# Performance work log

Hardware: AMD Instinct MI355X
Metric: run time of the kernel (lower is better)

Reference implementation:

```python
import jax, jax.numpy as jnp
import numpy as np

D_MODEL = 512
N_HEAD = 8
D_HEAD = D_MODEL // N_HEAD


def setup_inputs() -> dict:
    key = jax.random.key(0)
    ks = jax.random.split(key, 8)
    B, S, T = 4, 512, 32
    src = jax.random.normal(ks[0], (B, S, D_MODEL), dtype=jnp.float32)
    tgt = jax.random.normal(ks[1], (B, S, T, D_MODEL), dtype=jnp.float32)
    tgt_padding_mask = jax.random.bernoulli(ks[2], 0.1, (B, S, T))
    scale = 1.0 / np.sqrt(D_MODEL)
    in_proj_weight = jax.random.uniform(ks[3], (3 * D_MODEL, D_MODEL), dtype=jnp.float32, minval=-scale, maxval=scale)
    in_proj_bias = jnp.zeros((3 * D_MODEL,), dtype=jnp.float32)
    out_proj_weight = jax.random.uniform(ks[4], (D_MODEL, D_MODEL), dtype=jnp.float32, minval=-scale, maxval=scale)
    out_proj_bias = jnp.zeros((D_MODEL,), dtype=jnp.float32)
    return {
        "src": src,
        "tgt": tgt,
        "tgt_padding_mask": tgt_padding_mask,
        "in_proj_weight": in_proj_weight,
        "in_proj_bias": in_proj_bias,
        "out_proj_weight": out_proj_weight,
        "out_proj_bias": out_proj_bias,
    }


def reference(src, tgt, tgt_padding_mask, in_proj_weight, in_proj_bias, out_proj_weight, out_proj_bias):
    # KNN-style cross attention branch (tgt is [B, S, T, D]).
    B, S, _ = src.shape
    T = tgt.shape[-2]
    w_src, w_tgt = in_proj_weight[:D_MODEL], in_proj_weight[D_MODEL:]
    b_src, b_tgt = in_proj_bias[:D_MODEL], in_proj_bias[D_MODEL:]

    q = src @ w_src.T + b_src                      # [B, S, D]
    kv = tgt @ w_tgt.T + b_tgt                     # [B, S, T, 2D]
    k, v = kv[..., :D_MODEL], kv[..., D_MODEL:]

    # mask handling: drop the mask for queries with no valid tgt, zero them later
    attn_invalid = tgt_padding_mask                # [B, S, T]
    mask_no_tgt_valid = jnp.all(attn_invalid, axis=-1)           # [B, S]
    attn_invalid = attn_invalid & ~mask_no_tgt_valid[..., None]

    q = q.reshape(B, S, N_HEAD, D_HEAD)            # [B, S, H, Dh]
    k = k.reshape(B, S, T, N_HEAD, D_HEAD)
    v = v.reshape(B, S, T, N_HEAD, D_HEAD)

    attn = jnp.einsum("bshd,bsthd->bhst", q, k)    # [B, H, S, T]
    attn = jnp.where(attn_invalid[:, None], -jnp.inf, attn)
    attn = jax.nn.softmax(attn / jnp.sqrt(jnp.asarray(D_HEAD, attn.dtype)), axis=-1)

    out = jnp.einsum("bhst,bsthd->bshd", attn, v).reshape(B, S, D_MODEL)
    out = out @ out_proj_weight.T + out_proj_bias
    out = jnp.where(mask_no_tgt_valid[..., None], 0.0, out)
    return out
```

## Files before the change

### kernel.cpp

```cpp
#include <hip/hip_runtime.h>
#include <hip/hip_bf16.h>

#define BS_   2048
#define T_    32
#define DM_   512

typedef __attribute__((ext_vector_type(8))) short frag8;
typedef __attribute__((ext_vector_type(4))) float f32x4;

__device__ __forceinline__ short f2s(float v) {
    return __builtin_bit_cast(short, __float2bfloat16(v));
}
__device__ __forceinline__ float s2f(short x) {
    return __builtin_bit_cast(float, (unsigned)(unsigned short)x << 16);
}
__device__ __forceinline__ void stv(float* p, float v)          { *p = v; }
__device__ __forceinline__ void stv(__hip_bfloat16* p, float v) { *p = __float2bfloat16(v); }

__device__ __forceinline__ void gl_lds16(const __hip_bfloat16* g, __hip_bfloat16* l) {
    __builtin_amdgcn_global_load_lds(
        (const __attribute__((address_space(1))) unsigned int*)g,
        (__attribute__((address_space(3))) unsigned int*)l, 16, 0, 0);
}

__global__ __launch_bounds__(256)
void prep(const float* __restrict__ ipw, const float* __restrict__ opw,
          const float* __restrict__ src,
          __hip_bfloat16* __restrict__ ipw_bf, __hip_bfloat16* __restrict__ opw_bf,
          __hip_bfloat16* __restrict__ src_bf, __hip_bfloat16* __restrict__ Tk)
{
    __shared__ __hip_bfloat16 tile[64][65];
    int b = blockIdx.x;
    if (b < 2048) {
        int g = b * 256 + threadIdx.x;
        const float4* in; ushort4* out; int off;
        if (g < 196608)      { in = (const float4*)ipw; out = (ushort4*)ipw_bf; off = g; }
        else if (g < 262144) { in = (const float4*)opw; out = (ushort4*)opw_bf; off = g - 196608; }
        else                 { in = (const float4*)src; out = (ushort4*)src_bf; off = g - 262144; }
        float4 v = in[off];
        ushort4 o;
        o.x = (unsigned short)f2s(v.x); o.y = (unsigned short)f2s(v.y);
        o.z = (unsigned short)f2s(v.z); o.w = (unsigned short)f2s(v.w);
        out[off] = o;
    } else {
        int bb = b - 2048;
        int bx = bb & 15, by = bb >> 4;
        int tid = threadIdx.x;
        const float* sp = ipw + (size_t)512 * 512;
#pragma unroll
        for (int i = 0; i < 16; ++i) {
            int idx = i * 256 + tid;
            int r = idx >> 6, c = idx & 63;
            tile[r][c] = __float2bfloat16(sp[(size_t)(bx * 64 + r) * 512 + by * 64 + c]);
        }
        __syncthreads();
#pragma unroll
        for (int i = 0; i < 16; ++i) {
            int idx = i * 256 + tid;
            int rr = idx >> 6, cc = idx & 63;
            Tk[(size_t)(by * 64 + rr) * 1024 + bx * 64 + cc] = tile[cc][rr];
        }
    }
}

template<typename OUTT>
__global__ __launch_bounds__(256)
void gemm128(const __hip_bfloat16* __restrict__ A,
             const __hip_bfloat16* __restrict__ W,
             const float* __restrict__ bias,
             OUTT* __restrict__ C,
             const int* __restrict__ zrow,
             int M, int N, int K)
{
    __shared__ __hip_bfloat16 sA[128 * 64];
    __shared__ __hip_bfloat16 sB[128 * 64];

    int tid  = threadIdx.x;
    int lane = tid & 63;
    int wave = tid >> 6;
    int tn = blockIdx.x, tm = blockIdx.y;
    int wm = wave >> 1, wn = wave & 1;

    const __hip_bfloat16* Ab = A + (size_t)tm * 128 * K;
    const __hip_bfloat16* Wb = W + (size_t)tn * 128 * K;

    f32x4 acc[4][4];
#pragma unroll
    for (int i = 0; i < 4; ++i)
#pragma unroll
        for (int j = 0; j < 4; ++j) acc[i][j] = {0.f, 0.f, 0.f, 0.f};

    int wbase = (tid & ~63) * 8;
    int m  = lane & 15;
    int q  = lane >> 4;
    int sw = (m & 7) * 8;
    int trow = tid >> 3;
    int tcb  = ((tid & 7) ^ (trow & 7)) * 8;

    for (int k0 = 0; k0 < K; k0 += 64) {
#pragma unroll
        for (int i = 0; i < 4; ++i)
            gl_lds16(Ab + (size_t)(i * 32 + trow) * K + k0 + tcb, &sA[i * 2048 + wbase]);
#pragma unroll
        for (int i = 0; i < 4; ++i)
            gl_lds16(Wb + (size_t)(i * 32 + trow) * K + k0 + tcb, &sB[i * 2048 + wbase]);
        __syncthreads();
#pragma unroll
        for (int ki = 0; ki < 2; ++ki) {
            frag8 af[4], bf[4];
#pragma unroll
            for (int i = 0; i < 4; ++i)
                af[i] = *(const frag8*)&sA[(wm * 64 + i * 16 + m) * 64 + (((ki * 4 + q) * 8) ^ sw)];
#pragma unroll
            for (int j = 0; j < 4; ++j)
                bf[j] = *(const frag8*)&sB[(wn * 64 + j * 16 + m) * 64 + (((ki * 4 + q) * 8) ^ sw)];
#pragma unroll
            for (int i = 0; i < 4; ++i)
#pragma unroll
                for (int j = 0; j < 4; ++j)
                    acc[i][j] = __builtin_amdgcn_mfma_f32_16x16x32_bf16(
                        af[i], bf[j], acc[i][j], 0, 0, 0);
        }
        __syncthreads();
    }

    int rb = (lane >> 4) * 4;
#pragma unroll
    for (int j = 0; j < 4; ++j) {
        int   col = tn * 128 + wn * 64 + j * 16 + m;
        float bv  = bias[col];
#pragma unroll
        for (int i = 0; i < 4; ++i) {
            int row0 = tm * 128 + wm * 64 + i * 16 + rb;
#pragma unroll
            for (int t = 0; t < 4; ++t) {
                int   row = row0 + t;
                float v   = acc[i][j][t] + bv;
                if (zrow && zrow[row]) v = 0.f;
                stv(&C[(size_t)row * N + col], v);
            }
        }
    }
}

__global__ __launch_bounds__(256)
void gemm_bt_g(const __hip_bfloat16* __restrict__ A, int lda, long astr,
               const __hip_bfloat16* __restrict__ W, int ldw, long wstr,
               const float* __restrict__ bias, int bstr,
               __hip_bfloat16* __restrict__ C, int ldc, long cstr,
               int M, int N, int K)
{
    int z = blockIdx.y;
    A += (size_t)z * astr;  W += (size_t)z * wstr;  C += (size_t)z * cstr;
    int bcol0 = z * bstr;

    int wave = blockIdx.x * 4 + (threadIdx.x >> 6);
    int lane = threadIdx.x & 63;
    int ntn  = N / 32;
    int tm = wave / ntn, tn = wave - tm * ntn;
    if (tm * 32 >= M) return;

    int r  = lane & 15;
    int kq = (lane >> 4) << 3;
    const __hip_bfloat16* Ap = A + (size_t)(tm * 32 + r) * lda + kq;
    const __hip_bfloat16* Wp = W + (size_t)(tn * 32 + r) * ldw + kq;

    f32x4 acc[2][2];
#pragma unroll
    for (int i = 0; i < 2; ++i)
#pragma unroll
        for (int j = 0; j < 2; ++j) acc[i][j] = {0.f, 0.f, 0.f, 0.f};

    for (int k0 = 0; k0 < K; k0 += 32) {
        frag8 a[2], b[2];
#pragma unroll
        for (int i = 0; i < 2; ++i) a[i] = *(const frag8*)(Ap + (size_t)i * 16 * lda + k0);
#pragma unroll
        for (int j = 0; j < 2; ++j) b[j] = *(const frag8*)(Wp + (size_t)j * 16 * ldw + k0);
#pragma unroll
        for (int i = 0; i < 2; ++i)
#pragma unroll
            for (int j = 0; j < 2; ++j)
                acc[i][j] = __builtin_amdgcn_mfma_f32_16x16x32_bf16(a[i], b[j], acc[i][j], 0, 0, 0);
    }

    int rb = (lane >> 4) * 4;
#pragma unroll
    for (int j = 0; j < 2; ++j) {
        int   col = tn * 32 + j * 16 + r;
        float bv  = bias ? bias[bcol0 + col] : 0.f;
#pragma unroll
        for (int i = 0; i < 2; ++i) {
            int row0 = tm * 32 + i * 16 + rb;
#pragma unroll
            for (int t = 0; t < 4; ++t)
                C[(size_t)(row0 + t) * ldc + col] =
                    __float2bfloat16(acc[i][j][t] + bv);
        }
    }
}

__global__ __launch_bounds__(256)
void fused_attn(const float* __restrict__ tgt,
                const __hip_bfloat16* __restrict__ qkh,
                const int* __restrict__ mask,
                __hip_bfloat16* __restrict__ tbar,
                int* __restrict__ zrow)
{
    int bs   = blockIdx.x;
    int tid  = threadIdx.x;
    int lane = tid & 63;
    int wv   = tid >> 6;
    int m    = lane & 15;
    int g4   = lane >> 4;

    __shared__ short sS[32 * 520];
    __shared__ short sTT[512 * 32];
    __shared__ short sQK[8 * 520];
    __shared__ int   sM[32];

    const float* tg = tgt + (size_t)bs * 32 * 512;
#pragma unroll
    for (int i = 0; i < 16; ++i) {
        int idx = i * 256 + tid;
        int row = idx >> 7, c4 = (idx & 127) * 4;
        float4 v = *(const float4*)(tg + (size_t)row * 512 + c4);
        ushort4 o;
        o.x = (unsigned short)f2s(v.x); o.y = (unsigned short)f2s(v.y);
        o.z = (unsigned short)f2s(v.z); o.w = (unsigned short)f2s(v.w);
        *(ushort4*)&sS[row * 520 + c4] = o;
    }
    const ushort4* qk4 = (const ushort4*)(qkh + (size_t)bs * 4096);
#pragma unroll
    for (int i = 0; i < 4; ++i) {
        int u = i * 256 + tid;
        int h = u >> 7, c4 = (u & 127) * 4;
        *(ushort4*)&sQK[h * 520 + c4] = qk4[u];
    }
    if (tid < 32) sM[tid] = mask[bs * 32 + tid];
    __syncthreads();

    {
        int rot = (tid >> 1) & 7;
#pragma unroll
        for (int cc = 0; cc < 2; ++cc) {
            int c = tid + cc * 256;
#pragma unroll
            for (int s = 0; s < 8; ++s) {
                int t0 = ((s + rot) & 7) * 4;
                ushort4 o;
                o.x = (unsigned short)sS[(t0 + 0) * 520 + c];
                o.y = (unsigned short)sS[(t0 + 1) * 520 + c];
                o.z = (unsigned short)sS[(t0 + 2) * 520 + c];
                o.w = (unsigned short)sS[(t0 + 3) * 520 + c];
                *(ushort4*)&sTT[c * 32 + t0] = o;
            }
        }
    }

    int mk0 = sM[m], mk1 = sM[16 + m];
    bool allm = __all((mk0 != 0) && (mk1 != 0));
    if (tid == 0) zrow[bs] = allm ? 1 : 0;

    f32x4 acc0 = {0.f,0.f,0.f,0.f}, acc1 = {0.f,0.f,0.f,0.f};
    {
        const short* qb  = &sQK[(m & 7) * 520 + g4 * 8];
        const short* t0p = &sS[m * 520 + g4 * 8];
        const short* t1p = t0p + 16 * 520;
#pragma unroll
        for (int k0 = 0; k0 < 512; k0 += 32) {
            frag8 af = *(const frag8*)(qb + k0);
            frag8 b0 = *(const frag8*)(t0p + k0);
            frag8 b1 = *(const frag8*)(t1p + k0);
            acc0 = __builtin_amdgcn_mfma_f32_16x16x32_bf16(af, b0, acc0, 0, 0, 0);
            acc1 = __builtin_amdgcn_mfma_f32_16x16x32_bf16(af, b1, acc1, 0, 0, 0);
        }
    }

    float p0v[4], p1v[4];
#pragma unroll
    for (int r = 0; r < 4; ++r) {
        float s0 = acc0[r] * 0.125f, s1 = acc1[r] * 0.125f;
        if (!allm) {
            if (mk0) s0 = -__builtin_inff();
            if (mk1) s1 = -__builtin_inff();
        }
        float mx = fmaxf(s0, s1);
#pragma unroll
        for (int off = 1; off < 16; off <<= 1) mx = fmaxf(mx, __shfl_xor(mx, off));
        float e0 = __expf(s0 - mx), e1 = __expf(s1 - mx);
        float sm = e0 + e1;
#pragma unroll
        for (int off = 1; off < 16; off <<= 1) sm += __shfl_xor(sm, off);
        float inv = 1.f / sm;
        p0v[r] = e0 * inv; p1v[r] = e1 * inv;
    }

    __syncthreads();

    short* sPw = &sQK[0] + wv * 512;
    if (g4 < 2) {
#pragma unroll
        for (int r = 0; r < 4; ++r) {
            int h = g4 * 4 + r;
            short h0 = f2s(p0v[r]);
            short h1 = f2s(p1v[r]);
            sPw[h * 32 + m]            = h0;
            sPw[h * 32 + 16 + m]       = h1;
            sPw[256 + h * 32 + m]      = f2s(p0v[r] - s2f(h0));
            sPw[256 + h * 32 + 16 + m] = f2s(p1v[r] - s2f(h1));
        }
    }
    __syncthreads();

    frag8 paH = *(const frag8*)(sPw + (m & 7) * 32 + g4 * 8);
    frag8 paL = *(const frag8*)(sPw + 256 + (m & 7) * 32 + g4 * 8);

    short* sO = &sS[0];
#pragma unroll
    for (int ci = 0; ci < 8; ++ci) {
        int cg = wv * 8 + ci;
        frag8 vb = *(const frag8*)(&sTT[(cg * 16 + m) * 32 + g4 * 8]);
        f32x4 d = {0.f,0.f,0.f,0.f};
        d = __builtin_amdgcn_mfma_f32_16x16x32_bf16(paH, vb, d, 0, 0, 0);
        d = __builtin_amdgcn_mfma_f32_16x16x32_bf16(paL, vb, d, 0, 0, 0);
        if (g4 < 2) {
#pragma unroll
            for (int r = 0; r < 4; ++r)
                sO[(g4 * 4 + r) * 512 + cg * 16 + m] = f2s(d[r]);
        }
    }
    __syncthreads();

    ushort4* dst = (ushort4*)(tbar + (size_t)bs * 4096);
    const ushort4* so4 = (const ushort4*)sO;
#pragma unroll
    for (int i = 0; i < 4; ++i)
        dst[i * 256 + tid] = so4[i * 256 + tid];
}

extern "C" void kernel_launch(void* const* d_in, const int* in_sizes, int n_in,
                              void* d_out, int out_size, void* d_ws, size_t ws_size,
                              hipStream_t stream)
{
    const float* src  = (const float*)d_in[0];
    const float* tgt  = (const float*)d_in[1];
    const int*   mask = (const int*)d_in[2];
    const float* ipw  = (const float*)d_in[3];
    const float* ipb  = (const float*)d_in[4];
    const float* opw  = (const float*)d_in[5];
    const float* opb  = (const float*)d_in[6];
    float*       out  = (float*)d_out;

    char* ws = (char*)d_ws;
    __hip_bfloat16* src_bf = (__hip_bfloat16*)(ws);
    __hip_bfloat16* ipw_bf = (__hip_bfloat16*)(ws + ((size_t)2 << 20));
    __hip_bfloat16* opw_bf = (__hip_bfloat16*)(ws + ((size_t)2 << 20) + 1536 * 512 * 2);
    __hip_bfloat16* q_bf   = (__hip_bfloat16*)(ws + ((size_t)4 << 20));
    __hip_bfloat16* Tk     = (__hip_bfloat16*)(ws + ((size_t)6 << 20));
    __hip_bfloat16* qkh    = (__hip_bfloat16*)(ws + ((size_t)8 << 20));
    __hip_bfloat16* tbar   = (__hip_bfloat16*)(ws + ((size_t)24 << 20));
    __hip_bfloat16* ao_bf  = (__hip_bfloat16*)(ws + ((size_t)40 << 20));
    int*            zrow   = (int*)(ws + ((size_t)42 << 20));

    prep<<<2176, 256, 0, stream>>>(ipw, opw, src, ipw_bf, opw_bf, src_bf, Tk);

    gemm128<__hip_bfloat16><<<dim3(4, 16), 256, 0, stream>>>(
        src_bf, ipw_bf, ipb, q_bf, nullptr, BS_, DM_, DM_);

    gemm_bt_g<<<dim3(256, 8), 256, 0, stream>>>(
        q_bf, 512, 64,  Tk, 1024, 64,  nullptr, 0,
        qkh, 4096, 512,  BS_, 512, 64);

    fused_attn<<<BS_, 256, 0, stream>>>(tgt, qkh, mask, tbar, zrow);

    gemm_bt_g<<<dim3(32, 8), 256, 0, stream>>>(
        tbar, 4096, 512,  ipw_bf + (size_t)1024 * 512, 512, (long)64 * 512,
        ipb + 1024, 64,
        ao_bf, 512, 64,  BS_, 64, 512);

    gemm128<float><<<dim3(4, 16), 256, 0, stream>>>(
        ao_bf, opw_bf, opb, out, zrow, BS_, DM_, DM_);
}
```

Before: 273.7 us.

## Fuse all stages into one cooperative persistent kernel with grid syncs

Replaces the six separate launches with a single cooperative kernel of 512 blocks that runs prep, Q projection, QK, attention, value projection and output projection as stages separated by grid-wide syncs. The 128x128 GEMM tiles shrink to 64x64 so there are enough blocks, and the zero-row flag is recomputed from the mask in the output epilogue rather than written by the attention stage. This targets launch overhead and inter-kernel gaps, but adds grid barriers and forces attention to run with only 512 resident blocks looping four times, with roughly 74KB of LDS per block, which limits occupancy. If the cooperative launch fails, the code falls back to separate kernels.

```diff
diff --git a/kernel.cpp b/kernel.cpp
--- a/kernel.cpp
+++ b/kernel.cpp
@@ -1,9 +1,9 @@
 #include <hip/hip_runtime.h>
 #include <hip/hip_bf16.h>
-
-#define BS_   2048
-#define T_    32
-#define DM_   512
+#include <hip/hip_cooperative_groups.h>
+
+namespace cg = cooperative_groups;
+
 
 typedef __attribute__((ext_vector_type(8))) short frag8;
 typedef __attribute__((ext_vector_type(4))) float f32x4;
@@ -23,143 +23,138 @@
         (__attribute__((address_space(3))) unsigned int*)l, 16, 0, 0);
 }
 
-__global__ __launch_bounds__(256)
-void prep(const float* __restrict__ ipw, const float* __restrict__ opw,
-          const float* __restrict__ src,
-          __hip_bfloat16* __restrict__ ipw_bf, __hip_bfloat16* __restrict__ opw_bf,
-          __hip_bfloat16* __restrict__ src_bf, __hip_bfloat16* __restrict__ Tk)
-{
-    __shared__ __hip_bfloat16 tile[64][65];
-    int b = blockIdx.x;
-    if (b < 2048) {
-        int g = b * 256 + threadIdx.x;
-        const float4* in; ushort4* out; int off;
-        if (g < 196608)      { in = (const float4*)ipw; out = (ushort4*)ipw_bf; off = g; }
-        else if (g < 262144) { in = (const float4*)opw; out = (ushort4*)opw_bf; off = g - 196608; }
-        else                 { in = (const float4*)src; out = (ushort4*)src_bf; off = g - 262144; }
+__device__ __forceinline__
+void stage_prep(int b, int tid, char* smem,
+                const float* __restrict__ ipw, const float* __restrict__ opw,
+                const float* __restrict__ src,
+                __hip_bfloat16* __restrict__ ipw_bf, __hip_bfloat16* __restrict__ opw_bf,
+                __hip_bfloat16* __restrict__ src_bf, __hip_bfloat16* __restrict__ Tk)
+{
+#pragma unroll
+    for (int i = 0; i < 4; ++i) {
+        int g = b * 1024 + i * 256 + tid;
+        const float4* in; ushort4* o4; int off;
+        if (g < 196608)      { in = (const float4*)ipw; o4 = (ushort4*)ipw_bf; off = g; }
+        else if (g < 262144) { in = (const float4*)opw; o4 = (ushort4*)opw_bf; off = g - 196608; }
+        else                 { in = (const float4*)src; o4 = (ushort4*)src_bf; off = g - 262144; }
         float4 v = in[off];
         ushort4 o;
         o.x = (unsigned short)f2s(v.x); o.y = (unsigned short)f2s(v.y);
         o.z = (unsigned short)f2s(v.z); o.w = (unsigned short)f2s(v.w);
-        out[off] = o;
-    } else {
-        int bb = b - 2048;
-        int bx = bb & 15, by = bb >> 4;
-        int tid = threadIdx.x;
+        o4[off] = o;
+    }
+    if (b < 128) {
+        short (*tile)[65] = (short(*)[65])smem;
+        int bx = b & 15, by = b >> 4;
         const float* sp = ipw + (size_t)512 * 512;
 #pragma unroll
         for (int i = 0; i < 16; ++i) {
             int idx = i * 256 + tid;
             int r = idx >> 6, c = idx & 63;
-            tile[r][c] = __float2bfloat16(sp[(size_t)(bx * 64 + r) * 512 + by * 64 + c]);
+            tile[r][c] = f2s(sp[(size_t)(bx * 64 + r) * 512 + by * 64 + c]);
         }
         __syncthreads();
+        short* Tks = (short*)Tk;
 #pragma unroll
         for (int i = 0; i < 16; ++i) {
             int idx = i * 256 + tid;
             int rr = idx >> 6, cc = idx & 63;
-            Tk[(size_t)(by * 64 + rr) * 1024 + bx * 64 + cc] = tile[cc][rr];
-        }
+            Tks[(size_t)(by * 64 + rr) * 1024 + bx * 64 + cc] = tile[cc][rr];
+        }
+        __syncthreads();
     }
 }
 
 template<typename OUTT>
-__global__ __launch_bounds__(256)
-void gemm128(const __hip_bfloat16* __restrict__ A,
-             const __hip_bfloat16* __restrict__ W,
-             const float* __restrict__ bias,
-             OUTT* __restrict__ C,
-             const int* __restrict__ zrow,
-             int M, int N, int K)
-{
-    __shared__ __hip_bfloat16 sA[128 * 64];
-    __shared__ __hip_bfloat16 sB[128 * 64];
-
-    int tid  = threadIdx.x;
-    int lane = tid & 63;
-    int wave = tid >> 6;
-    int tn = blockIdx.x, tm = blockIdx.y;
-    int wm = wave >> 1, wn = wave & 1;
-
-    const __hip_bfloat16* Ab = A + (size_t)tm * 128 * K;
-    const __hip_bfloat16* Wb = W + (size_t)tn * 128 * K;
-
-    f32x4 acc[4][4];
-#pragma unroll
-    for (int i = 0; i < 4; ++i)
-#pragma unroll
-        for (int j = 0; j < 4; ++j) acc[i][j] = {0.f, 0.f, 0.f, 0.f};
+__device__ __forceinline__
+void gemm64_dev(const __hip_bfloat16* __restrict__ A, const __hip_bfloat16* __restrict__ W,
+                const float* __restrict__ bias, OUTT* __restrict__ C,
+                const int* __restrict__ zmask,
+                int N, int K, int tm, int tn, char* smem, int tid)
+{
+    short* sA = (short*)smem;
+    short* sB = sA + 4096;
+    int lane = tid & 63, w = tid >> 6;
+    int wm = w >> 1, wn = w & 1;
+    const __hip_bfloat16* Ab = A + (size_t)tm * 64 * K;
+    const __hip_bfloat16* Wb = W + (size_t)tn * 64 * K;
+
+    f32x4 acc[2][2];
+#pragma unroll
+    for (int i = 0; i < 2; ++i)
+#pragma unroll
+        for (int j = 0; j < 2; ++j) acc[i][j] = {0.f, 0.f, 0.f, 0.f};
 
     int wbase = (tid & ~63) * 8;
-    int m  = lane & 15;
-    int q  = lane >> 4;
+    int m = lane & 15, q = lane >> 4;
     int sw = (m & 7) * 8;
     int trow = tid >> 3;
     int tcb  = ((tid & 7) ^ (trow & 7)) * 8;
 
     for (int k0 = 0; k0 < K; k0 += 64) {
-#pragma unroll
-        for (int i = 0; i < 4; ++i)
-            gl_lds16(Ab + (size_t)(i * 32 + trow) * K + k0 + tcb, &sA[i * 2048 + wbase]);
-#pragma unroll
-        for (int i = 0; i < 4; ++i)
-            gl_lds16(Wb + (size_t)(i * 32 + trow) * K + k0 + tcb, &sB[i * 2048 + wbase]);
+        gl_lds16(Ab + (size_t)trow * K + k0 + tcb,        (__hip_bfloat16*)&sA[wbase]);
+        gl_lds16(Ab + (size_t)(32 + trow) * K + k0 + tcb, (__hip_bfloat16*)&sA[2048 + wbase]);
+        gl_lds16(Wb + (size_t)trow * K + k0 + tcb,        (__hip_bfloat16*)&sB[wbase]);
+        gl_lds16(Wb + (size_t)(32 + trow) * K + k0 + tcb, (__hip_bfloat16*)&sB[2048 + wbase]);
         __syncthreads();
 #pragma unroll
         for (int ki = 0; ki < 2; ++ki) {
-            frag8 af[4], bf[4];
-#pragma unroll
-            for (int i = 0; i < 4; ++i)
-                af[i] = *(const frag8*)&sA[(wm * 64 + i * 16 + m) * 64 + (((ki * 4 + q) * 8) ^ sw)];
-#pragma unroll
-            for (int j = 0; j < 4; ++j)
-                bf[j] = *(const frag8*)&sB[(wn * 64 + j * 16 + m) * 64 + (((ki * 4 + q) * 8) ^ sw)];
-#pragma unroll
-            for (int i = 0; i < 4; ++i)
-#pragma unroll
-                for (int j = 0; j < 4; ++j)
+            frag8 af[2], bf2[2];
+#pragma unroll
+            for (int i = 0; i < 2; ++i)
+                af[i] = *(const frag8*)&sA[(wm * 32 + i * 16 + m) * 64 + ((ki * 32 + q * 8) ^ sw)];
+#pragma unroll
+            for (int j = 0; j < 2; ++j)
+                bf2[j] = *(const frag8*)&sB[(wn * 32 + j * 16 + m) * 64 + ((ki * 32 + q * 8) ^ sw)];
+#pragma unroll
+            for (int i = 0; i < 2; ++i)
+#pragma unroll
+                for (int j = 0; j < 2; ++j)
                     acc[i][j] = __builtin_amdgcn_mfma_f32_16x16x32_bf16(
-                        af[i], bf[j], acc[i][j], 0, 0, 0);
+                        af[i], bf2[j], acc[i][j], 0, 0, 0);
         }
         __syncthreads();
     }
 
-    int rb = (lane >> 4) * 4;
-#pragma unroll
-    for (int j = 0; j < 4; ++j) {
-        int   col = tn * 128 + wn * 64 + j * 16 + m;
+    int rb = q * 4;
+    bool zr[2][4] = {{false,false,false,false},{false,false,false,false}};
+    if (zmask) {
+#pragma unroll
+        for (int i = 0; i < 2; ++i)
+#pragma unroll
+            for (int t = 0; t < 4; ++t) {
+                int row = tm * 64 + wm * 32 + i * 16 + rb + t;
+                const uint4* mp = (const uint4*)(zmask + (size_t)row * 32);
+                unsigned a = 0xffffffffu;
+#pragma unroll
+                for (int u = 0; u < 8; ++u) { uint4 v = mp[u]; a &= v.x & v.y & v.z & v.w; }
+                zr[i][t] = (a != 0u);
+            }
+    }
+#pragma unroll
+    for (int j = 0; j < 2; ++j) {
+        int   col = tn * 64 + wn * 32 + j * 16 + m;
         float bv  = bias[col];
 #pragma unroll
-        for (int i = 0; i < 4; ++i) {
-            int row0 = tm * 128 + wm * 64 + i * 16 + rb;
+        for (int i = 0; i < 2; ++i) {
+            int row0 = tm * 64 + wm * 32 + i * 16 + rb;
 #pragma unroll
             for (int t = 0; t < 4; ++t) {
-                int   row = row0 + t;
-                float v   = acc[i][j][t] + bv;
-                if (zrow && zrow[row]) v = 0.f;
-                stv(&C[(size_t)row * N + col], v);
+                float v = acc[i][j][t] + bv;
+                if (zr[i][t]) v = 0.f;
+                stv(&C[(size_t)(row0 + t) * N + col], v);
             }
         }
     }
 }
 
-__global__ __launch_bounds__(256)
-void gemm_bt_g(const __hip_bfloat16* __restrict__ A, int lda, long astr,
-               const __hip_bfloat16* __restrict__ W, int ldw, long wstr,
-               const float* __restrict__ bias, int bstr,
-               __hip_bfloat16* __restrict__ C, int ldc, long cstr,
-               int M, int N, int K)
-{
-    int z = blockIdx.y;
-    A += (size_t)z * astr;  W += (size_t)z * wstr;  C += (size_t)z * cstr;
-    int bcol0 = z * bstr;
-
-    int wave = blockIdx.x * 4 + (threadIdx.x >> 6);
-    int lane = threadIdx.x & 63;
-    int ntn  = N / 32;
-    int tm = wave / ntn, tn = wave - tm * ntn;
-    if (tm * 32 >= M) return;
-
+__device__ __forceinline__
+void gemm_bt_wave(const __hip_bfloat16* __restrict__ A, int lda,
+                  const __hip_bfloat16* __restrict__ W, int ldw,
+                  const float* __restrict__ bias, int bc0,
+                  __hip_bfloat16* __restrict__ C, int ldc,
+                  int K, int tm, int tn, int lane)
+{
     int r  = lane & 15;
     int kq = (lane >> 4) << 3;
     const __hip_bfloat16* Ap = A + (size_t)(tm * 32 + r) * lda + kq;
@@ -188,36 +183,27 @@
 #pragma unroll
     for (int j = 0; j < 2; ++j) {
         int   col = tn * 32 + j * 16 + r;
-        float bv  = bias ? bias[bcol0 + col] : 0.f;
+        float bv  = bias ? bias[bc0 + col] : 0.f;
 #pragma unroll
         for (int i = 0; i < 2; ++i) {
             int row0 = tm * 32 + i * 16 + rb;
 #pragma unroll
             for (int t = 0; t < 4; ++t)
-                C[(size_t)(row0 + t) * ldc + col] =
-                    __float2bfloat16(acc[i][j][t] + bv);
-        }
-    }
-}
-
-__global__ __launch_bounds__(256)
-void fused_attn(const float* __restrict__ tgt,
-                const __hip_bfloat16* __restrict__ qkh,
-                const int* __restrict__ mask,
-                __hip_bfloat16* __restrict__ tbar,
-                int* __restrict__ zrow)
-{
-    int bs   = blockIdx.x;
-    int tid  = threadIdx.x;
-    int lane = tid & 63;
-    int wv   = tid >> 6;
-    int m    = lane & 15;
-    int g4   = lane >> 4;
-
-    __shared__ short sS[32 * 520];
-    __shared__ short sTT[512 * 32];
-    __shared__ short sQK[8 * 520];
-    __shared__ int   sM[32];
+                C[(size_t)(row0 + t) * ldc + col] = __float2bfloat16(acc[i][j][t] + bv);
+        }
+    }
+}
+
+__device__ __forceinline__
+void attn_dev(int bs, char* smem, const float* __restrict__ tgt,
+              const __hip_bfloat16* __restrict__ qkh, const int* __restrict__ mask,
+              __hip_bfloat16* __restrict__ tbar, int tid)
+{
+    int lane = tid & 63, wv = tid >> 6, m = lane & 15, g4 = lane >> 4;
+    short* sS  = (short*)smem;
+    short* sTT = sS + 16640;
+    short* sQK = sTT + 16384;
+    int*   sM  = (int*)(sQK + 4160);
 
     const float* tg = tgt + (size_t)bs * 32 * 512;
 #pragma unroll
@@ -257,10 +243,8 @@
             }
         }
     }
-
     int mk0 = sM[m], mk1 = sM[16 + m];
     bool allm = __all((mk0 != 0) && (mk1 != 0));
-    if (tid == 0) zrow[bs] = allm ? 1 : 0;
 
     f32x4 acc0 = {0.f,0.f,0.f,0.f}, acc1 = {0.f,0.f,0.f,0.f};
     {
@@ -276,7 +260,6 @@
             acc1 = __builtin_amdgcn_mfma_f32_16x16x32_bf16(af, b1, acc1, 0, 0, 0);
         }
     }
-
     float p0v[4], p1v[4];
 #pragma unroll
     for (int r = 0; r < 4; ++r) {
@@ -295,16 +278,13 @@
         float inv = 1.f / sm;
         p0v[r] = e0 * inv; p1v[r] = e1 * inv;
     }
-
     __syncthreads();
-
-    short* sPw = &sQK[0] + wv * 512;
+    short* sPw = sQK + wv * 512;
     if (g4 < 2) {
 #pragma unroll
         for (int r = 0; r < 4; ++r) {
             int h = g4 * 4 + r;
-            short h0 = f2s(p0v[r]);
-            short h1 = f2s(p1v[r]);
+            short h0 = f2s(p0v[r]), h1 = f2s(p1v[r]);
             sPw[h * 32 + m]            = h0;
             sPw[h * 32 + 16 + m]       = h1;
             sPw[256 + h * 32 + m]      = f2s(p0v[r] - s2f(h0));
@@ -312,11 +292,10 @@
         }
     }
     __syncthreads();
-
     frag8 paH = *(const frag8*)(sPw + (m & 7) * 32 + g4 * 8);
     frag8 paL = *(const frag8*)(sPw + 256 + (m & 7) * 32 + g4 * 8);
 
-    short* sO = &sS[0];
+    short* sO = sS;
 #pragma unroll
     for (int ci = 0; ci < 8; ++ci) {
         int cg = wv * 8 + ci;
@@ -331,12 +310,120 @@
         }
     }
     __syncthreads();
-
     ushort4* dst = (ushort4*)(tbar + (size_t)bs * 4096);
     const ushort4* so4 = (const ushort4*)sO;
 #pragma unroll
     for (int i = 0; i < 4; ++i)
         dst[i * 256 + tid] = so4[i * 256 + tid];
+}
+
+__global__ __launch_bounds__(256, 2)
+void fused_all(const float* src, const float* tgt, const int* mask,
+               const float* ipw, const float* ipb,
+               const float* opw, const float* opb, float* out,
+               __hip_bfloat16* src_bf, __hip_bfloat16* ipw_bf,
+               __hip_bfloat16* opw_bf, __hip_bfloat16* q_bf,
+               __hip_bfloat16* Tk, __hip_bfloat16* qkh,
+               __hip_bfloat16* tbar, __hip_bfloat16* ao_bf)
+{
+    cg::grid_group gg = cg::this_grid();
+    __shared__ __align__(16) char smem[74496];
+    int b = blockIdx.x, tid = threadIdx.x;
+    int lane = tid & 63, wv = tid >> 6;
+
+    stage_prep(b, tid, smem, ipw, opw, src, ipw_bf, opw_bf, src_bf, Tk);
+    gg.sync();
+
+    if (b < 256)
+        gemm64_dev<__hip_bfloat16>(src_bf, ipw_bf, ipb, q_bf, nullptr,
+                                   512, 512, b >> 3, b & 7, smem, tid);
+    gg.sync();
+
+#pragma unroll
+    for (int rep = 0; rep < 4; ++rep) {
+        int t = b * 4 + wv + rep * 2048;
+        int z = t >> 10, loc = t & 1023;
+        gemm_bt_wave(q_bf + z * 64, 512, Tk + z * 64, 1024, nullptr, 0,
+                     qkh + (size_t)z * 512, 4096, 64, loc >> 4, loc & 15, lane);
+    }
+    gg.sync();
+
+    for (int rep = 0; rep < 4; ++rep) {
+        attn_dev(b + rep * 512, smem, tgt, qkh, mask, tbar, tid);
+        __syncthreads();
+    }
+    gg.sync();
+
+    {
+        int gw = b * 4 + wv;
+        if (gw < 1024) {
+            int z = gw >> 7, loc = gw & 127;
+            gemm_bt_wave(tbar + (size_t)z * 512, 4096,
+                         ipw_bf + (size_t)(1024 + z * 64) * 512, 512,
+                         ipb + 1024, z * 64,
+                         ao_bf + z * 64, 512, 512, loc >> 1, loc & 1, lane);
+        }
+    }
+    gg.sync();
+
+    if (b < 256)
+        gemm64_dev<float>(ao_bf, opw_bf, opb, out, mask,
+                          512, 512, b >> 3, b & 7, smem, tid);
+}
+
+__global__ __launch_bounds__(256)
+void k_prep(const float* ipw, const float* opw, const float* src,
+            __hip_bfloat16* ipw_bf, __hip_bfloat16* opw_bf,
+            __hip_bfloat16* src_bf, __hip_bfloat16* Tk)
+{
+    __shared__ __align__(16) char smem[8320];
+    stage_prep(blockIdx.x, threadIdx.x, smem, ipw, opw, src, ipw_bf, opw_bf, src_bf, Tk);
+}
+__global__ __launch_bounds__(256)
+void k_q(const __hip_bfloat16* src_bf, const __hip_bfloat16* ipw_bf,
+         const float* ipb, __hip_bfloat16* q_bf)
+{
+    __shared__ __align__(16) char smem[16384];
+    int b = blockIdx.x;
+    gemm64_dev<__hip_bfloat16>(src_bf, ipw_bf, ipb, q_bf, nullptr,
+                               512, 512, b >> 3, b & 7, smem, threadIdx.x);
+}
+__global__ __launch_bounds__(256)
+void k_qk(const __hip_bfloat16* q_bf, const __hip_bfloat16* Tk, __hip_bfloat16* qkh)
+{
+    int tid = threadIdx.x;
+    int t = blockIdx.x * 4 + (tid >> 6);
+    int z = t >> 10, loc = t & 1023;
+    gemm_bt_wave(q_bf + z * 64, 512, Tk + z * 64, 1024, nullptr, 0,
+                 qkh + (size_t)z * 512, 4096, 64, loc >> 4, loc & 15, tid & 63);
+}
+__global__ __launch_bounds__(256)
+void k_attn(const float* tgt, const __hip_bfloat16* qkh, const int* mask,
+            __hip_bfloat16* tbar)
+{
+    __shared__ __align__(16) char smem[74496];
+    attn_dev(blockIdx.x, smem, tgt, qkh, mask, tbar, threadIdx.x);
+}
+__global__ __launch_bounds__(256)
+void k_ao(const __hip_bfloat16* tbar, const __hip_bfloat16* ipw_bf,
+          const float* ipb, __hip_bfloat16* ao_bf)
+{
+    int tid = threadIdx.x;
+    int gw = blockIdx.x * 4 + (tid >> 6);
+    int z = gw >> 7, loc = gw & 127;
+    gemm_bt_wave(tbar + (size_t)z * 512, 4096,
+                 ipw_bf + (size_t)(1024 + z * 64) * 512, 512,
+                 ipb + 1024, z * 64, ao_bf + z * 64, 512, 512,
+                 loc >> 1, loc & 1, tid & 63);
+}
+__global__ __launch_bounds__(256)
+void k_out(const __hip_bfloat16* ao_bf, const __hip_bfloat16* opw_bf,
+           const float* opb, float* out, const int* mask)
+{
+    __shared__ __align__(16) char smem[16384];
+    int b = blockIdx.x;
+    gemm64_dev<float>(ao_bf, opw_bf, opb, out, mask,
+                      512, 512, b >> 3, b & 7, smem, threadIdx.x);
 }
 
 extern "C" void kernel_launch(void* const* d_in, const int* in_sizes, int n_in,
@@ -361,24 +448,22 @@
     __hip_bfloat16* qkh    = (__hip_bfloat16*)(ws + ((size_t)8 << 20));
     __hip_bfloat16* tbar   = (__hip_bfloat16*)(ws + ((size_t)24 << 20));
     __hip_bfloat16* ao_bf  = (__hip_bfloat16*)(ws + ((size_t)40 << 20));
-    int*            zrow   = (int*)(ws + ((size_t)42 << 20));
-
-    prep<<<2176, 256, 0, stream>>>(ipw, opw, src, ipw_bf, opw_bf, src_bf, Tk);
-
-    gemm128<__hip_bfloat16><<<dim3(4, 16), 256, 0, stream>>>(
-        src_bf, ipw_bf, ipb, q_bf, nullptr, BS_, DM_, DM_);
-
-    gemm_bt_g<<<dim3(256, 8), 256, 0, stream>>>(
-        q_bf, 512, 64,  Tk, 1024, 64,  nullptr, 0,
-        qkh, 4096, 512,  BS_, 512, 64);
-
-    fused_attn<<<BS_, 256, 0, stream>>>(tgt, qkh, mask, tbar, zrow);
-
-    gemm_bt_g<<<dim3(32, 8), 256, 0, stream>>>(
-        tbar, 4096, 512,  ipw_bf + (size_t)1024 * 512, 512, (long)64 * 512,
-        ipb + 1024, 64,
-        ao_bf, 512, 64,  BS_, 64, 512);
-
-    gemm128<float><<<dim3(4, 16), 256, 0, stream>>>(
-        ao_bf, opw_bf, opb, out, zrow, BS_, DM_, DM_);
-}
+
+    void* args[16] = {
+        (void*)&src, (void*)&tgt, (void*)&mask, (void*)&ipw, (void*)&ipb,
+        (void*)&opw, (void*)&opb, (void*)&out,
+        (void*)&src_bf, (void*)&ipw_bf, (void*)&opw_bf, (void*)&q_bf,
+        (void*)&Tk, (void*)&qkh, (void*)&tbar, (void*)&ao_bf
+    };
+    hipError_t e = hipLaunchCooperativeKernel((const void*)fused_all,
+                                              dim3(512), dim3(256),
+                                              (void**)args, 0, stream);
+    if (e != hipSuccess) {
+        k_prep<<<512, 256, 0, stream>>>(ipw, opw, src, ipw_bf, opw_bf, src_bf, Tk);
+        k_q   <<<256, 256, 0, stream>>>(src_bf, ipw_bf, ipb, q_bf);
+        k_qk  <<<2048, 256, 0, stream>>>(q_bf, Tk, qkh);
+        k_attn<<<2048, 256, 0, stream>>>(tgt, qkh, mask, tbar);
+        k_ao  <<<256, 256, 0, stream>>>(tbar, ipw_bf, ipb, ao_bf);
+        k_out <<<256, 256, 0, stream>>>(ao_bf, opw_bf, opb, out, mask);
+    }
+}
```

New measurement: 543.7 us. 98.6% more time.
